# Kernel optimization log

Hardware: AMD Instinct MI355X
Metric: run time of the kernel (lower is better)

Reference implementation:

```python
import jax, jax.numpy as jnp
import numpy as np


def conv3d(x, w, b=None):
    # x: (N,C,D,H,W), w: (O,I,3,3,3), stride 1, padding 1 == SAME
    y = jax.lax.conv_general_dilated(x, w, (1, 1, 1), 'SAME',
                                     dimension_numbers=('NCDHW', 'OIDHW', 'NCDHW'))
    if b is not None:
        y = y + b[None, :, None, None, None]
    return y


def grid_sample_3d(vol, gx, gy, gz):
    # vol: (B,D,H,W); gx/gy/gz: normalized coords in [-1,1], shape (B,D,H,W)
    # trilinear, zeros padding, align_corners=True (old torch default)
    B, D, H, W = vol.shape
    ix = (gx + 1.0) * 0.5 * (W - 1)
    iy = (gy + 1.0) * 0.5 * (H - 1)
    iz = (gz + 1.0) * 0.5 * (D - 1)
    x0f, y0f, z0f = jnp.floor(ix), jnp.floor(iy), jnp.floor(iz)
    tx, ty, tz = ix - x0f, iy - y0f, iz - z0f
    x0 = x0f.astype(jnp.int32)
    y0 = y0f.astype(jnp.int32)
    z0 = z0f.astype(jnp.int32)
    vol_flat = vol.reshape(B, D * H * W)
    out = jnp.zeros_like(vol)
    for dz in (0, 1):
        for dy in (0, 1):
            for dx in (0, 1):
                xc, yc, zc = x0 + dx, y0 + dy, z0 + dz
                w = ((tx if dx else 1.0 - tx) * (ty if dy else 1.0 - ty)
                     * (tz if dz else 1.0 - tz))
                inb = ((xc >= 0) & (xc < W) & (yc >= 0) & (yc < H)
                       & (zc >= 0) & (zc < D))
                idx = ((jnp.clip(zc, 0, D - 1) * H + jnp.clip(yc, 0, H - 1)) * W
                       + jnp.clip(xc, 0, W - 1))
                val = jnp.take_along_axis(vol_flat, idx.reshape(B, -1), axis=1)
                val = val.reshape(B, D, H, W) * inb.astype(vol.dtype)
                out = out + w * val
    return out


def setup_inputs() -> dict:
    key = jax.random.key(0)
    k1, k2, k3, k4 = jax.random.split(key, 4)
    B, C, Cout, S = 2, 32, 64, 64
    x = jax.random.normal(k1, (B, C, S, S, S), dtype=jnp.float32)
    w_off = jax.random.normal(k2, (3 * C, C, 3, 3, 3), dtype=jnp.float32) * 0.0005
    w_reg = jax.random.normal(k3, (Cout, C, 3, 3, 3), dtype=jnp.float32) * 0.05
    b_reg = jax.random.normal(k4, (Cout,), dtype=jnp.float32) * 0.05
    return {"x": x, "w_off": w_off, "w_reg": w_reg, "b_reg": b_reg}


def reference(x, w_off, w_reg, b_reg):
    B, C, D, H, W = x.shape
    offset = conv3d(x, w_off)  # (B, 3C, D, H, W)
    off_w, off_h, _ = jnp.split(offset, 3, axis=1)
    # NOTE: original code has offset_d = offset_h (faithful bug)
    off_d = off_h
    off_w = off_w.reshape(B * C, D, H, W)
    off_h = off_h.reshape(B * C, D, H, W)
    off_d = off_d.reshape(B * C, D, H, W)
    # np.meshgrid default 'xy' indexing: shapes (H, W, D) -> requires D==H==W
    gw, gh, gd = np.meshgrid(np.linspace(-1, 1, W), np.linspace(-1, 1, H),
                             np.linspace(-1, 1, D))
    grid_w = jnp.asarray(gw, dtype=x.dtype)
    grid_h = jnp.asarray(gh, dtype=x.dtype)
    grid_d = jnp.asarray(gd, dtype=x.dtype)
    off_w = off_w + grid_w
    off_h = off_h + grid_h
    off_d = off_d + grid_d
    vol = x.reshape(B * C, D, H, W)
    # torch grid stack order: (offset_h, offset_w, offset_d) -> (x, y, z)
    sampled = grid_sample_3d(vol, off_h, off_w, off_d)
    sampled = sampled.reshape(B, C, D, H, W)
    return conv3d(sampled, w_reg, b_reg)
```

## Files before the change

### kernel.cpp

```cpp
#include <hip/hip_runtime.h>
#include <cstddef>

#define S 64
#define VOL (64*64*64)
#define CIN 32

typedef __attribute__((ext_vector_type(8))) short bf16x8;
typedef __attribute__((ext_vector_type(4))) float floatx4;

struct __attribute__((packed, aligned(4))) fpair { float x, y; };

__device__ __forceinline__ unsigned short f2bf(float f) {
    union { float f; unsigned u; } v; v.f = f;
    unsigned r = v.u + 0x7fffu + ((v.u >> 16) & 1u);
    return (unsigned short)(r >> 16);
}
__device__ __forceinline__ float bf2f(unsigned short h) {
    union { unsigned u; float f; } v; v.u = ((unsigned)h) << 16;
    return v.f;
}
__device__ __forceinline__ int iclamp(int v, int lo, int hi) {
    return v < lo ? lo : (v > hi ? hi : v);
}

__device__ __forceinline__ void gload_lds16(const void* g, void* l) {
    __builtin_amdgcn_global_load_lds(
        (const __attribute__((address_space(1))) void*)g,
        (__attribute__((address_space(3))) void*)l, 16, 0, 0);
}

__global__ void prep_w_kernel(const float* __restrict__ w_off,
                              const float* __restrict__ w_reg,
                              unsigned short* __restrict__ wt1,
                              unsigned short* __restrict__ wt2) {
    int i = blockIdx.x * 256 + threadIdx.x;
    if (i >= 27 * 64 * 32) return;
    int ci = i & 31;
    int co = (i >> 5) & 63;
    int tap = i >> 11;
    wt1[i] = f2bf(w_off[(co * 32 + ci) * 27 + tap]);
    wt2[i] = f2bf(w_reg[(co * 32 + ci) * 27 + tap]);
}

__global__ __launch_bounds__(256)
void prepack_kernel(const float* __restrict__ x, unsigned* __restrict__ xb) {
    const unsigned id = blockIdx.x * 256 + threadIdx.x;
    const int b   = id >> 18;
    const int pos = id & (VOL - 1);
    const float* sp = x + (size_t)b * 32 * VOL + pos;
    float v[32];
#pragma unroll
    for (int c = 0; c < 32; ++c) v[c] = sp[(size_t)c * VOL];
    unsigned* dp = xb + (size_t)id * 16;
#pragma unroll
    for (int i = 0; i < 4; ++i) {
        uint4 pk;
        pk.x = (unsigned)f2bf(v[i*8+0]) | ((unsigned)f2bf(v[i*8+1]) << 16);
        pk.y = (unsigned)f2bf(v[i*8+2]) | ((unsigned)f2bf(v[i*8+3]) << 16);
        pk.z = (unsigned)f2bf(v[i*8+4]) | ((unsigned)f2bf(v[i*8+5]) << 16);
        pk.w = (unsigned)f2bf(v[i*8+6]) | ((unsigned)f2bf(v[i*8+7]) << 16);
        *(uint4*)(dp + i*4) = pk;
    }
}

template <bool WRITE_OFF>
__global__ __launch_bounds__(256, 2)
void conv_mfma_kernel(const unsigned short* __restrict__ src,
                      const unsigned short* __restrict__ wt,
                      const float* __restrict__ bias,
                      void* __restrict__ dstv) {
    __shared__ unsigned short lds[16 * 64 * 32];

    const int d0 = blockIdx.x * 2;
    const int h0 = blockIdx.y * 2;
    const int b  = blockIdx.z;
    const int t  = threadIdx.x;
    const int lane = t & 63;
    const int wv   = t >> 6;

    const int sl = lane >> 2;
    const int js = (lane & 3) ^ ((lane >> 3) & 3);
    const char* sbase = (const char*)src + (size_t)b * VOL * 64;
#pragma unroll
    for (int rr2 = 0; rr2 < 4; ++rr2) {
        const int rowi = (wv << 2) + rr2;
        const int z = d0 - 1 + (rowi >> 2);
        const int y = h0 - 1 + (rowi & 3);
        char* ldsrow = (char*)lds + (rowi << 12);
        if (((unsigned)z < 64u) && ((unsigned)y < 64u)) {
            const char* gb = sbase + ((size_t)(z * 4096 + y * 64)) * 64
                           + (sl << 6) + (js << 4);
#pragma unroll
            for (int k = 0; k < 4; ++k)
                gload_lds16(gb + (k << 10), ldsrow + (k << 10));
        } else {
            const uint4 z4 = make_uint4(0, 0, 0, 0);
#pragma unroll
            for (int k = 0; k < 4; ++k)
                *(uint4*)(ldsrow + (k << 10) + (lane << 4)) = z4;
        }
    }
    __syncthreads();

    const int r    = lane & 15;
    const int q    = lane >> 4;
    const int dd   = wv >> 1;
    const int hh   = wv & 1;

    int P[4][3];
#pragma unroll
    for (int nt = 0; nt < 4; ++nt)
#pragma unroll
        for (int kw = 0; kw < 3; ++kw) {
            const int s  = nt * 16 + r + kw - 1;
            const int sc = s & 63;
            P[nt][kw] = (sc << 6) + ((q ^ ((sc >> 1) & 3)) << 4);
        }

    floatx4 acc[4][4];
#pragma unroll
    for (int mt = 0; mt < 4; ++mt)
#pragma unroll
        for (int nt = 0; nt < 4; ++nt)
#pragma unroll
            for (int rg = 0; rg < 4; ++rg) acc[mt][nt][rg] = 0.f;

    const bf16x8 z8 = {0, 0, 0, 0, 0, 0, 0, 0};

#pragma unroll
    for (int tap = 0; tap < 27; ++tap) {
        const int kd = tap / 9;
        const int kh = (tap % 9) / 3;
        const int kw = tap % 3;
        const int rowb = ((((dd + kd) << 2) + hh + kh) << 12);

        bf16x8 afr[4];
#pragma unroll
        for (int mt = 0; mt < 4; ++mt)
            afr[mt] = *(const bf16x8*)&wt[tap * 2048 + (mt * 16 + r) * 32 + q * 8];

        bf16x8 bfr[4];
#pragma unroll
        for (int nt = 0; nt < 4; ++nt)
            bfr[nt] = *(const bf16x8*)((const char*)lds + rowb + P[nt][kw]);

        if (kw == 0) { if (r == 0)  bfr[0] = z8; }
        if (kw == 2) { if (r == 15) bfr[3] = z8; }

#pragma unroll
        for (int mt = 0; mt < 4; ++mt)
#pragma unroll
            for (int nt = 0; nt < 4; ++nt)
                acc[mt][nt] = __builtin_amdgcn_mfma_f32_16x16x32_bf16(
                                  afr[mt], bfr[nt], acc[mt][nt], 0, 0, 0);
    }

    const int dw = (d0 + dd) * 4096 + (h0 + hh) * 64;
    if (WRITE_OFF) {
        unsigned* dst = (unsigned*)dstv + (size_t)b * VOL * 32;
#pragma unroll
        for (int mt = 0; mt < 2; ++mt) {
#pragma unroll
            for (int nt = 0; nt < 4; ++nt) {
                const int pos = dw + nt * 16 + r;
                uint4 pk;
                pk.x = (unsigned)f2bf(acc[mt][nt][0]) | ((unsigned)f2bf(acc[mt+2][nt][0]) << 16);
                pk.y = (unsigned)f2bf(acc[mt][nt][1]) | ((unsigned)f2bf(acc[mt+2][nt][1]) << 16);
                pk.z = (unsigned)f2bf(acc[mt][nt][2]) | ((unsigned)f2bf(acc[mt+2][nt][2]) << 16);
                pk.w = (unsigned)f2bf(acc[mt][nt][3]) | ((unsigned)f2bf(acc[mt+2][nt][3]) << 16);
                *(uint4*)(dst + (size_t)pos * 32 + mt * 16 + q * 4) = pk;
            }
        }
    } else {
#pragma unroll
        for (int mt = 0; mt < 4; ++mt) {
#pragma unroll
            for (int nt = 0; nt < 4; ++nt) {
#pragma unroll
                for (int rg = 0; rg < 4; ++rg) {
                    const int co  = mt * 16 + q * 4 + rg;
                    const int pos = dw + nt * 16 + r;
                    ((float*)dstv)[((size_t)(b * 64 + co)) * VOL + pos]
                        = acc[mt][nt][rg] + bias[co];
                }
            }
        }
    }
}

__global__ __launch_bounds__(256, 4)
void gather_kernel(const float* __restrict__ x,
                   const unsigned* __restrict__ off32,
                   unsigned* __restrict__ sampled) {
    const int t = threadIdx.x;
    const unsigned gid = blockIdx.x;
    const int b   = gid >> 10;
    const int j   = gid & 1023;
    const int wt4 = j & 3;
    const int dt  = (j >> 2) & 3;
    const int h   = j >> 4;
    const int d_i = t & 15;
    const int w_i = t >> 4;
    const int d = dt * 16 + d_i;
    const int w = wt4 * 16 + w_i;
    const int p = d * 4096 + h * 64 + w;

    const unsigned* op = off32 + ((size_t)(b * VOL + p)) * 32;
    const float* xb_ = x + (size_t)b * 32 * VOL;
    const float fd = (float)d, fh = (float)h, fw = (float)w;

    float outv[32];
#pragma unroll
    for (int cq = 0; cq < 8; ++cq) {
        const uint4 o4 = *(const uint4*)(op + cq * 4);
        const unsigned oarr[4] = {o4.x, o4.y, o4.z, o4.w};
#pragma unroll
        for (int ce = 0; ce < 4; ++ce) {
            const int c = cq * 4 + ce;
            const unsigned ow = oarr[ce];
            const float offw = bf2f((unsigned short)(ow & 0xffffu));
            const float offh = bf2f((unsigned short)(ow >> 16));
            const float* vol = xb_ + (size_t)c * VOL;

            const float ix = offh * 31.5f + fd;
            const float iy = offw * 31.5f + fh;
            const float iz = offh * 31.5f + fw;

            const float x0f = floorf(ix), y0f = floorf(iy), z0f = floorf(iz);
            const float tx = ix - x0f, ty = iy - y0f, tz = iz - z0f;
            const int ix0 = (int)x0f, iy0 = (int)y0f, iz0 = (int)z0f;

            const int bx0 = iclamp(ix0, 0, 62);
            const bool sel = (ix0 == bx0);
            const float w0x = ((unsigned)ix0 < 64u)       ? (1.f - tx) : 0.f;
            const float w1x = ((unsigned)(ix0 + 1) < 64u) ? tx         : 0.f;

            float out = 0.f;
#pragma unroll
            for (int dz = 0; dz < 2; ++dz) {
                const int zc = iz0 + dz;
                const bool zok = ((unsigned)zc < 64u);
                const int zcc = iclamp(zc, 0, 63);
                const float wz = dz ? tz : 1.f - tz;
#pragma unroll
                for (int dy = 0; dy < 2; ++dy) {
                    const int yc = iy0 + dy;
                    const bool yok = ((unsigned)yc < 64u);
                    const int ycc = iclamp(yc, 0, 63);
                    const float wzy = (zok && yok) ? wz * (dy ? ty : 1.f - ty) : 0.f;

                    const fpair vp = *(const fpair*)&vol[(zcc * 64 + ycc) * 64 + bx0];
                    const float v0 = sel ? vp.x : vp.y;
                    const float v1 = sel ? vp.y : vp.x;
                    out += wzy * (w0x * v0 + w1x * v1);
                }
            }
            outv[c] = out;
        }
    }

    unsigned* sp = sampled + ((size_t)(b * VOL + p)) * 16;
#pragma unroll
    for (int i = 0; i < 4; ++i) {
        uint4 pk;
        pk.x = (unsigned)f2bf(outv[i*8+0]) | ((unsigned)f2bf(outv[i*8+1]) << 16);
        pk.y = (unsigned)f2bf(outv[i*8+2]) | ((unsigned)f2bf(outv[i*8+3]) << 16);
        pk.z = (unsigned)f2bf(outv[i*8+4]) | ((unsigned)f2bf(outv[i*8+5]) << 16);
        pk.w = (unsigned)f2bf(outv[i*8+6]) | ((unsigned)f2bf(outv[i*8+7]) << 16);
        *(uint4*)(sp + i*4) = pk;
    }
}

extern "C" void kernel_launch(void* const* d_in, const int* in_sizes, int n_in,
                              void* d_out, int out_size, void* d_ws, size_t ws_size,
                              hipStream_t stream) {
    (void)in_sizes; (void)n_in; (void)out_size; (void)ws_size;
    const float* x     = (const float*)d_in[0];
    const float* w_off = (const float*)d_in[1];
    const float* w_reg = (const float*)d_in[2];
    const float* b_reg = (const float*)d_in[3];
    float* out = (float*)d_out;

    unsigned* off32 = (unsigned*)d_ws;
    unsigned* buf   = off32 + (size_t)2 * VOL * 32;
    unsigned short* wt1 = (unsigned short*)(buf + (size_t)2 * VOL * 16);
    unsigned short* wt2 = wt1 + 27 * 64 * 32;

    prep_w_kernel<<<216, 256, 0, stream>>>(w_off, w_reg, wt1, wt2);
    prepack_kernel<<<2048, 256, 0, stream>>>(x, buf);

    dim3 cgrid(32, 32, 2);
    conv_mfma_kernel<true><<<cgrid, 256, 0, stream>>>(
        (const unsigned short*)buf, wt1, nullptr, (void*)off32);

    gather_kernel<<<2048, 256, 0, stream>>>(x, off32, buf);

    conv_mfma_kernel<false><<<cgrid, 256, 0, stream>>>(
        (const unsigned short*)buf, wt2, b_reg, (void*)out);
}
```

Baseline: 445.8 us.

## Stage prepack stores via LDS, split conv barrier, and shrink gather register footprint

Three separate changes. Prepack now stages its packed bf16 rows in a swizzled LDS buffer so the global writes become fully coalesced across the block. The conv kernel replaces its single barrier with a split wait: three waves wait for their own loads before tap 0, and the last wave's loads (the rows only needed from tap 18) are waited on later, overlapping that load with early MFMA work. Gather processes channels in groups of eight with a non-unrolled loop and writes each packed group immediately, cutting register use so occupancy can rise to 8 blocks per CU, at the cost of less instruction-level parallelism per thread.

```diff
diff --git a/kernel.cpp b/kernel.cpp
--- a/kernel.cpp
+++ b/kernel.cpp
@@ -43,15 +43,17 @@
 }
 
 __global__ __launch_bounds__(256)
-void prepack_kernel(const float* __restrict__ x, unsigned* __restrict__ xb) {
-    const unsigned id = blockIdx.x * 256 + threadIdx.x;
+void prepack_kernel(const float* __restrict__ x, uint4* __restrict__ xb4) {
+    __shared__ uint4 pbuf[1024];
+    const int t = threadIdx.x;
+    const unsigned id0 = blockIdx.x * 256;
+    const unsigned id  = id0 + t;
     const int b   = id >> 18;
     const int pos = id & (VOL - 1);
     const float* sp = x + (size_t)b * 32 * VOL + pos;
     float v[32];
 #pragma unroll
     for (int c = 0; c < 32; ++c) v[c] = sp[(size_t)c * VOL];
-    unsigned* dp = xb + (size_t)id * 16;
 #pragma unroll
     for (int i = 0; i < 4; ++i) {
         uint4 pk;
@@ -59,7 +61,15 @@
         pk.y = (unsigned)f2bf(v[i*8+2]) | ((unsigned)f2bf(v[i*8+3]) << 16);
         pk.z = (unsigned)f2bf(v[i*8+4]) | ((unsigned)f2bf(v[i*8+5]) << 16);
         pk.w = (unsigned)f2bf(v[i*8+6]) | ((unsigned)f2bf(v[i*8+7]) << 16);
-        *(uint4*)(dp + i*4) = pk;
+        pbuf[t * 4 + (i ^ (t & 3))] = pk;
+    }
+    __syncthreads();
+#pragma unroll
+    for (int i = 0; i < 4; ++i) {
+        const int g  = i * 256 + t;
+        const int ch = g & 3;
+        const int lw = g >> 2;
+        xb4[(size_t)id0 * 4 + g] = pbuf[lw * 4 + (ch ^ (lw & 3))];
     }
 }
 
@@ -100,7 +110,6 @@
                 *(uint4*)(ldsrow + (k << 10) + (lane << 4)) = z4;
         }
     }
-    __syncthreads();
 
     const int r    = lane & 15;
     const int q    = lane >> 4;
@@ -125,10 +134,20 @@
 #pragma unroll
             for (int rg = 0; rg < 4; ++rg) acc[mt][nt][rg] = 0.f;
 
+    asm volatile("s_waitcnt lgkmcnt(0)" ::: "memory");
+    if (wv < 3) asm volatile("s_waitcnt vmcnt(0)" ::: "memory");
+    __builtin_amdgcn_s_barrier();
+    __builtin_amdgcn_sched_barrier(0);
+
     const bf16x8 z8 = {0, 0, 0, 0, 0, 0, 0, 0};
 
 #pragma unroll
     for (int tap = 0; tap < 27; ++tap) {
+        if (tap == 18) {
+            if (wv == 3) asm volatile("s_waitcnt vmcnt(0)" ::: "memory");
+            __builtin_amdgcn_s_barrier();
+            __builtin_amdgcn_sched_barrier(0);
+        }
         const int kd = tap / 9;
         const int kh = (tap % 9) / 3;
         const int kw = tap % 3;
@@ -188,10 +207,10 @@
     }
 }
 
-__global__ __launch_bounds__(256, 4)
+__global__ __launch_bounds__(256, 8)
 void gather_kernel(const float* __restrict__ x,
-                   const unsigned* __restrict__ off32,
-                   unsigned* __restrict__ sampled) {
+                   const uint4* __restrict__ off4,
+                   uint4* __restrict__ samp4) {
     const int t = threadIdx.x;
     const unsigned gid = blockIdx.x;
     const int b   = gid >> 10;
@@ -205,18 +224,20 @@
     const int w = wt4 * 16 + w_i;
     const int p = d * 4096 + h * 64 + w;
 
-    const unsigned* op = off32 + ((size_t)(b * VOL + p)) * 32;
+    const uint4* op = off4 + ((size_t)b * VOL + p) * 8;
+    uint4* sp       = samp4 + ((size_t)b * VOL + p) * 4;
     const float* xb_ = x + (size_t)b * 32 * VOL;
     const float fd = (float)d, fh = (float)h, fw = (float)w;
 
-    float outv[32];
-#pragma unroll
-    for (int cq = 0; cq < 8; ++cq) {
-        const uint4 o4 = *(const uint4*)(op + cq * 4);
-        const unsigned oarr[4] = {o4.x, o4.y, o4.z, o4.w};
-#pragma unroll
-        for (int ce = 0; ce < 4; ++ce) {
-            const int c = cq * 4 + ce;
+#pragma unroll 1
+    for (int g = 0; g < 4; ++g) {
+        const uint4 oA = op[g * 2 + 0];
+        const uint4 oB = op[g * 2 + 1];
+        const unsigned oarr[8] = {oA.x, oA.y, oA.z, oA.w, oB.x, oB.y, oB.z, oB.w};
+        float outv[8];
+#pragma unroll
+        for (int ce = 0; ce < 8; ++ce) {
+            const int c = g * 8 + ce;
             const unsigned ow = oarr[ce];
             const float offw = bf2f((unsigned short)(ow & 0xffffu));
             const float offh = bf2f((unsigned short)(ow >> 16));
@@ -255,19 +276,14 @@
                     out += wzy * (w0x * v0 + w1x * v1);
                 }
             }
-            outv[c] = out;
-        }
-    }
-
-    unsigned* sp = sampled + ((size_t)(b * VOL + p)) * 16;
-#pragma unroll
-    for (int i = 0; i < 4; ++i) {
+            outv[ce] = out;
+        }
         uint4 pk;
-        pk.x = (unsigned)f2bf(outv[i*8+0]) | ((unsigned)f2bf(outv[i*8+1]) << 16);
-        pk.y = (unsigned)f2bf(outv[i*8+2]) | ((unsigned)f2bf(outv[i*8+3]) << 16);
-        pk.z = (unsigned)f2bf(outv[i*8+4]) | ((unsigned)f2bf(outv[i*8+5]) << 16);
-        pk.w = (unsigned)f2bf(outv[i*8+6]) | ((unsigned)f2bf(outv[i*8+7]) << 16);
-        *(uint4*)(sp + i*4) = pk;
+        pk.x = (unsigned)f2bf(outv[0]) | ((unsigned)f2bf(outv[1]) << 16);
+        pk.y = (unsigned)f2bf(outv[2]) | ((unsigned)f2bf(outv[3]) << 16);
+        pk.z = (unsigned)f2bf(outv[4]) | ((unsigned)f2bf(outv[5]) << 16);
+        pk.w = (unsigned)f2bf(outv[6]) | ((unsigned)f2bf(outv[7]) << 16);
+        sp[g] = pk;
     }
 }
 
@@ -287,13 +303,13 @@
     unsigned short* wt2 = wt1 + 27 * 64 * 32;
 
     prep_w_kernel<<<216, 256, 0, stream>>>(w_off, w_reg, wt1, wt2);
-    prepack_kernel<<<2048, 256, 0, stream>>>(x, buf);
+    prepack_kernel<<<2048, 256, 0, stream>>>(x, (uint4*)buf);
 
     dim3 cgrid(32, 32, 2);
     conv_mfma_kernel<true><<<cgrid, 256, 0, stream>>>(
         (const unsigned short*)buf, wt1, nullptr, (void*)off32);
 
-    gather_kernel<<<2048, 256, 0, stream>>>(x, off32, buf);
+    gather_kernel<<<2048, 256, 0, stream>>>(x, (const uint4*)off32, (uint4*)buf);
 
     conv_mfma_kernel<false><<<cgrid, 256, 0, stream>>>(
         (const unsigned short*)buf, wt2, b_reg, (void*)out);
```

Measured after the change: 441.8 us. About the same (-0.9%).
